# Optimization experiments

Measured on AMD Instinct MI355X. Metric: run time of the kernel, lower is better.

Reference implementation:

```python
import jax, jax.numpy as jnp
import numpy as np

N_NODES = 100000
N_EDGES = 1200000
N_GRAPHS = 512
N_REL = 3
NUM_SHAPES = 16
NUM_COLORS = 16
NUM_CLASS = 10


def setup_inputs() -> dict:
    key = jax.random.key(0)
    ks = jax.random.split(key, 16)
    inp = {
        "x": jax.random.randint(ks[0], (N_NODES, 2), 0, NUM_SHAPES),
        "edge_index": jax.random.randint(ks[1], (2, N_EDGES), 0, N_NODES),
        "edge_type": jax.random.randint(ks[2], (N_EDGES,), 0, N_REL),
        "batch": jnp.sort(jax.random.randint(ks[3], (N_NODES,), 0, N_GRAPHS)),
        # parameters
        "se": jax.random.normal(ks[4], (NUM_SHAPES, 8), jnp.float32) * 0.1,
        "ce": jax.random.normal(ks[5], (NUM_COLORS, 8), jnp.float32) * 0.1,
        "pre_w": jax.random.normal(ks[6], (16, 32), jnp.float32) * 0.1,
        "pre_b": jnp.zeros((32,), jnp.float32),
        "w1": jax.random.normal(ks[7], (N_REL, 32, 64), jnp.float32) * 0.1,
        "root1": jax.random.normal(ks[8], (32, 64), jnp.float32) * 0.1,
        "b1": jnp.zeros((64,), jnp.float32),
        "w2": jax.random.normal(ks[9], (N_REL, 64, 64), jnp.float32) * 0.1,
        "root2": jax.random.normal(ks[10], (64, 64), jnp.float32) * 0.1,
        "b2": jnp.zeros((64,), jnp.float32),
        "cls_w": jax.random.normal(ks[11], (64, NUM_CLASS), jnp.float32) * 0.1,
        "cls_b": jnp.zeros((NUM_CLASS,), jnp.float32),
    }
    return inp


def _rgcn(h, src, dst, edge_type, weight, root, bias):
    # PyG RGCNConv with aggr='mean': out = x @ root + bias + sum_r mean_{edges of rel r}(x_j @ W_r)
    out = h @ root + bias
    for r in range(N_REL):
        mask = (edge_type == r)
        hr = h @ weight[r]                      # [N, out] transform-then-gather
        msg = jnp.where(mask[:, None], hr[src], 0.0)  # [E, out]
        agg = jax.ops.segment_sum(msg, dst, num_segments=N_NODES)
        cnt = jax.ops.segment_sum(mask.astype(h.dtype), dst, num_segments=N_NODES)
        out = out + agg / jnp.maximum(cnt, 1.0)[:, None]
    return out


def reference(x, edge_index, edge_type, batch, se, ce, pre_w, pre_b,
              w1, root1, b1, w2, root2, b2, cls_w, cls_b):
    h = jnp.concatenate([se[x[:, 0]], ce[x[:, 1]]], axis=1)  # [N,16]
    h = jax.nn.relu(h @ pre_w + pre_b)                        # [N,32]
    src, dst = edge_index[0], edge_index[1]
    h = jax.nn.relu(_rgcn(h, src, dst, edge_type, w1, root1, b1))  # [N,64]
    h = jax.nn.relu(_rgcn(h, src, dst, edge_type, w2, root2, b2))  # [N,64]
    # global mean pool over graph ids
    s = jax.ops.segment_sum(h, batch, num_segments=N_GRAPHS)
    c = jax.ops.segment_sum(jnp.ones((h.shape[0],), h.dtype), batch, num_segments=N_GRAPHS)
    g = s / jnp.maximum(c, 1.0)[:, None]                      # [G,64]
    return g @ cls_w + cls_b                                  # [G,num_class]
```

## Files before the change

kernel.cpp:

```cpp
#include <hip/hip_runtime.h>

#define NN 100000
#define NE 1200000
#define NG 512
#define NSEG (3 * NN)
#define NC 4
#define CHUNK 1024
#define NCHUNK ((NSEG + CHUNK - 1) / CHUNK)

typedef __bf16 bf16x8 __attribute__((ext_vector_type(8)));
typedef float f32x4 __attribute__((ext_vector_type(4)));

static constexpr size_t AGG_OFF   = 0;
static constexpr size_t AGG_BYTES = (size_t)NSEG * 32 * 4;
static constexpr size_t HIST_OFF  = AGG_OFF + AGG_BYTES;
static constexpr size_t START_OFF = HIST_OFF + (size_t)NC * NSEG * 4;
static constexpr size_t END_OFF   = START_OFF + (size_t)NSEG * 4;
static constexpr size_t COFF_OFF  = END_OFF + (size_t)NSEG * 4;
static constexpr size_t CSUM_OFF  = COFF_OFF + (size_t)NSEG * 4;
static constexpr size_t ESRC_OFF  = CSUM_OFF + 4096;
static constexpr size_t H1_OFF    = ESRC_OFF + (size_t)NE * 4;
static constexpr size_t H2_OFF    = H1_OFF + (size_t)NN * 64 * 2;
static constexpr size_t WT1H_OFF  = H2_OFF + (size_t)NN * 64 * 4;
static constexpr size_t WT1L_OFF  = WT1H_OFF + 64 * 128 * 2;
static constexpr size_t WT2H_OFF  = WT1L_OFF + 64 * 128 * 2;
static constexpr size_t WT2L_OFF  = WT2H_OFF + 64 * 256 * 2;
static constexpr size_t TAB_OFF   = WT2L_OFF + 64 * 256 * 2;
static constexpr size_t CB_OFF    = TAB_OFF + 256 * 32 * 4;
static constexpr size_t RS_OFF    = ((CB_OFF + NN + 15) / 16) * 16;

__device__ __forceinline__ void async_copy16(void* lds, const void* g) {
    __builtin_amdgcn_global_load_lds(
        (const __attribute__((address_space(1))) void*)g,
        (__attribute__((address_space(3))) void*)lds, 16, 0, 0);
}

__device__ __forceinline__ void prepw_elem(const float* root, const float* w,
                                           __bf16* wh, __bf16* wl, int cin, int t) {
    int kt = 4 * cin;
    if (t >= 64 * kt) return;
    int j = t / kt, k = t % kt;
    int sidx = k / cin, kk = k % cin;
    float v = (sidx == 0) ? root[kk * 64 + j]
                          : w[((size_t)(sidx - 1) * cin + kk) * 64 + j];
    __bf16 h = (__bf16)v;
    wh[t] = h;
    wl[t] = (__bf16)(v - (float)h);
}

#define RB_BASE 488
__global__ __launch_bounds__(256)
void k_rank_prep(const int* __restrict__ ei, const int* __restrict__ et,
                 int* __restrict__ hist4, unsigned int* __restrict__ rs,
                 const int* __restrict__ x, const float* __restrict__ se,
                 const float* __restrict__ ce, const float* __restrict__ pw,
                 const float* __restrict__ pb,
                 const float* __restrict__ root1, const float* __restrict__ w1,
                 const float* __restrict__ root2, const float* __restrict__ w2,
                 __bf16* __restrict__ wh1, __bf16* __restrict__ wl1,
                 __bf16* __restrict__ wh2, __bf16* __restrict__ wl2,
                 float* __restrict__ table, unsigned char* __restrict__ cb) {
    int b = blockIdx.x, t = threadIdx.x;
    if (b >= RB_BASE) {
        int e = (b - RB_BASE) * 256 + t;
        if (e >= NE) return;
        int d = ei[NE + e];
        int r = et[e];
        int seg = r * NN + d;
        int c = e & (NC - 1);
        unsigned int rank = (unsigned int)atomicAdd(&hist4[c * NSEG + seg], 1);
        rs[e] = (rank << 19) | (unsigned int)seg;
        return;
    }
    if (b < 32) {
        prepw_elem(root1, w1, wh1, wl1, 32, b * 256 + t);
    } else if (b < 96) {
        prepw_elem(root2, w2, wh2, wl2, 64, (b - 32) * 256 + t);
    } else if (b == 96) {
        __shared__ float sW[16 * 32];
        __shared__ float sB[32];
        for (int i = t; i < 512; i += 256) sW[i] = pw[i];
        if (t < 32) sB[t] = pb[t];
        __syncthreads();
        int cmb = t, s = cmb >> 4, c = cmb & 15;
        float in[16];
#pragma unroll
        for (int k = 0; k < 8; k++) in[k] = se[s * 8 + k];
#pragma unroll
        for (int k = 0; k < 8; k++) in[8 + k] = ce[c * 8 + k];
        float acc[32];
#pragma unroll
        for (int j = 0; j < 32; j++) acc[j] = sB[j];
#pragma unroll
        for (int k = 0; k < 16; k++) {
            float hv = in[k];
#pragma unroll
            for (int j = 0; j < 32; j++) acc[j] += hv * sW[k * 32 + j];
        }
        float* o = table + (size_t)cmb * 32;
#pragma unroll
        for (int j = 0; j < 32; j += 4)
            *(float4*)(o + j) = make_float4(fmaxf(acc[j], 0.f), fmaxf(acc[j + 1], 0.f),
                                            fmaxf(acc[j + 2], 0.f), fmaxf(acc[j + 3], 0.f));
    } else {
        int n = (b - 97) * 256 + t;
        if (n < NN) cb[n] = (unsigned char)(x[2 * n] * 16 + x[2 * n + 1]);
    }
}

__global__ __launch_bounds__(256)
void k_chunksum(const int* __restrict__ hist4, int* __restrict__ csum) {
    __shared__ int s[256];
    int b = blockIdx.x, t = threadIdx.x;
    int base = b * CHUNK + t * 4;
    int sum = 0;
#pragma unroll
    for (int k = 0; k < 4; k++) {
        int i = base + k;
        if (i < NSEG) {
#pragma unroll
            for (int c = 0; c < NC; c++) sum += hist4[c * NSEG + i];
        }
    }
    s[t] = sum;
    __syncthreads();
    for (int off = 128; off > 0; off >>= 1) {
        if (t < off) s[t] += s[t + off];
        __syncthreads();
    }
    if (t == 0) csum[b] = s[0];
}

__global__ __launch_bounds__(512)
void k_chunkscan(int* __restrict__ csum) {
    __shared__ int s[512];
    int t = threadIdx.x;
    int v = (t < NCHUNK) ? csum[t] : 0;
    s[t] = v;
    __syncthreads();
    for (int off = 1; off < 512; off <<= 1) {
        int x = (t >= off) ? s[t - off] : 0;
        __syncthreads();
        s[t] += x;
        __syncthreads();
    }
    if (t < NCHUNK) csum[t] = s[t] - v;
}

__global__ __launch_bounds__(256)
void k_localscan(const int* __restrict__ hist4, const int* __restrict__ csum,
                 int* __restrict__ start, int* __restrict__ end, int* __restrict__ coff) {
    __shared__ int s[256];
    int b = blockIdx.x, t = threadIdx.x;
    int base = b * CHUNK + t * 4;
    int tot[4], cofv[4];
    int s4 = 0;
#pragma unroll
    for (int k = 0; k < 4; k++) {
        int i = base + k;
        int c0 = 0, c1 = 0, c2 = 0, c3 = 0;
        if (i < NSEG) {
            c0 = hist4[0 * NSEG + i];
            c1 = hist4[1 * NSEG + i];
            c2 = hist4[2 * NSEG + i];
            c3 = hist4[3 * NSEG + i];
        }
        tot[k] = c0 + c1 + c2 + c3;
        cofv[k] = c0 | ((c0 + c1) << 8) | ((c0 + c1 + c2) << 16);
        s4 += tot[k];
    }
    s[t] = s4;
    __syncthreads();
    for (int off = 1; off < 256; off <<= 1) {
        int x = (t >= off) ? s[t - off] : 0;
        __syncthreads();
        s[t] += x;
        __syncthreads();
    }
    int excl = s[t] - s4 + csum[b];
#pragma unroll
    for (int k = 0; k < 4; k++) {
        int i = base + k;
        if (i < NSEG) {
            start[i] = excl;
            end[i] = excl + tot[k];
            coff[i] = cofv[k];
        }
        excl += tot[k];
    }
}

__global__ __launch_bounds__(256)
void k_fill2(const int* __restrict__ ei, const unsigned char* __restrict__ cb,
             const int* __restrict__ start, const int* __restrict__ coff,
             const unsigned int* __restrict__ rs, int* __restrict__ esrc) {
    int e = blockIdx.x * 256 + threadIdx.x;
    if (e >= NE) return;
    int s = ei[e];
    unsigned int v = rs[e];
    int seg = (int)(v & 0x7FFFFu);
    int rank = (int)(v >> 19);
    int c = e & (NC - 1);
    int off = c ? ((coff[seg] >> (8 * (c - 1))) & 0xFF) : 0;
    int pos = start[seg] + off + rank;
    esrc[pos] = s | ((int)cb[s] << 17);
}

__global__ __launch_bounds__(256)
void k_gather_t(const int* __restrict__ start, const int* __restrict__ end,
                const int* __restrict__ esrc, const float* __restrict__ table,
                float* __restrict__ agg) {
    int tid = blockIdx.x * 256 + threadIdx.x;
    int seg = tid >> 3;
    int p = tid & 7;
    if (seg >= NSEG) return;
    int st = start[seg], en = end[seg];
    float4 acc = make_float4(0.f, 0.f, 0.f, 0.f);
    int i = st;
    for (; i + 4 <= en; i += 4) {
        int v0 = esrc[i], v1 = esrc[i + 1], v2 = esrc[i + 2], v3 = esrc[i + 3];
        float4 a = *(const float4*)(table + ((v0 >> 17) & 0xFF) * 32 + p * 4);
        float4 b = *(const float4*)(table + ((v1 >> 17) & 0xFF) * 32 + p * 4);
        float4 c = *(const float4*)(table + ((v2 >> 17) & 0xFF) * 32 + p * 4);
        float4 d = *(const float4*)(table + ((v3 >> 17) & 0xFF) * 32 + p * 4);
        acc.x += (a.x + b.x) + (c.x + d.x);
        acc.y += (a.y + b.y) + (c.y + d.y);
        acc.z += (a.z + b.z) + (c.z + d.z);
        acc.w += (a.w + b.w) + (c.w + d.w);
    }
    for (; i < en; i++) {
        int v = esrc[i];
        float4 a = *(const float4*)(table + ((v >> 17) & 0xFF) * 32 + p * 4);
        acc.x += a.x; acc.y += a.y; acc.z += a.z; acc.w += a.w;
    }
    int c = en - st;
    float inv = 1.f / (float)(c > 1 ? c : 1);
    acc.x *= inv; acc.y *= inv; acc.z *= inv; acc.w *= inv;
    *(float4*)(agg + (size_t)seg * 32 + p * 4) = acc;
}

__global__ __launch_bounds__(256)
void k_gather64(const int* __restrict__ start, const int* __restrict__ end,
                const int* __restrict__ esrc, const __bf16* __restrict__ h,
                __bf16* __restrict__ agg) {
    int tid = blockIdx.x * 256 + threadIdx.x;
    int seg = tid >> 3;
    int p = tid & 7;
    if (seg >= NSEG) return;
    int st = start[seg], en = end[seg];
    float acc[8];
#pragma unroll
    for (int j = 0; j < 8; j++) acc[j] = 0.f;
    int i = st;
    for (; i + 4 <= en; i += 4) {
        int s0 = esrc[i] & 0x1FFFF, s1 = esrc[i + 1] & 0x1FFFF;
        int s2 = esrc[i + 2] & 0x1FFFF, s3 = esrc[i + 3] & 0x1FFFF;
        bf16x8 v0 = *(const bf16x8*)(h + (size_t)s0 * 64 + p * 8);
        bf16x8 v1 = *(const bf16x8*)(h + (size_t)s1 * 64 + p * 8);
        bf16x8 v2 = *(const bf16x8*)(h + (size_t)s2 * 64 + p * 8);
        bf16x8 v3 = *(const bf16x8*)(h + (size_t)s3 * 64 + p * 8);
#pragma unroll
        for (int j = 0; j < 8; j++)
            acc[j] += ((float)v0[j] + (float)v1[j]) + ((float)v2[j] + (float)v3[j]);
    }
    for (; i < en; i++) {
        int s = esrc[i] & 0x1FFFF;
        bf16x8 v = *(const bf16x8*)(h + (size_t)s * 64 + p * 8);
#pragma unroll
        for (int j = 0; j < 8; j++) acc[j] += (float)v[j];
    }
    int c = en - st;
    float inv = 1.f / (float)(c > 1 ? c : 1);
    bf16x8 o;
#pragma unroll
    for (int j = 0; j < 8; j++) o[j] = (__bf16)(acc[j] * inv);
    *(bf16x8*)(agg + (size_t)seg * 64 + p * 8) = o;
}

__device__ __forceinline__ void split8(float4 a0, float4 a1, bf16x8& hi, bf16x8& lo) {
    float v[8] = {a0.x, a0.y, a0.z, a0.w, a1.x, a1.y, a1.z, a1.w};
#pragma unroll
    for (int i = 0; i < 8; i++) {
        __bf16 h = (__bf16)v[i];
        hi[i] = h;
        lo[i] = (__bf16)(v[i] - (float)h);
    }
}

__global__ __launch_bounds__(256, 1)
void k_combine_l1(const float* __restrict__ table, const unsigned char* __restrict__ cb,
                  const float* __restrict__ agg,
                  const __bf16* __restrict__ wh, const __bf16* __restrict__ wl,
                  const float* __restrict__ bias, __bf16* __restrict__ h_out) {
    constexpr int KT = 128;
    __shared__ float sIN[64 * 64];
    __shared__ __bf16 sWH[64 * 64];
    __shared__ __bf16 sWL[64 * 64];

    const int tid = threadIdx.x;
    const int wave = tid >> 6;
    const int lane = tid & 63;
    const int cA = lane & 15;
    const int kg = lane >> 4;
    const int n0 = blockIdx.x * 64;

    f32x4 acc[4];
#pragma unroll
    for (int nb = 0; nb < 4; nb++) {
        float bv = bias[nb * 16 + cA];
        acc[nb][0] = bv; acc[nb][1] = bv; acc[nb][2] = bv; acc[nb][3] = bv;
    }

    for (int c = 0; c < 2; c++) {
        if (c) __syncthreads();
#pragma unroll
        for (int i = 0; i < 4; i++) {
            int F = tid + i * 256;
            int row = F >> 4, j = F & 15;
            int jor = j ^ (row & 7);
            int n = n0 + row; if (n > NN - 1) n = NN - 1;
            int sidx = 2 * c + (jor >> 3);
            int jj = jor & 7;
            const float* src = (sidx == 0)
                ? table + (size_t)cb[n] * 32 + jj * 4
                : agg + ((size_t)(sidx - 1) * NN + n) * 32 + jj * 4;
            async_copy16(sIN + (size_t)F * 4, src);
        }
#pragma unroll
        for (int i = 0; i < 2; i++) {
            int F = tid + i * 256;
            int col = F >> 3, s = F & 7;
            int sor = s ^ (col & 7);
            async_copy16(sWH + (size_t)F * 8, wh + (size_t)col * KT + c * 64 + sor * 8);
            async_copy16(sWL + (size_t)F * 8, wl + (size_t)col * KT + c * 64 + sor * 8);
        }
        __syncthreads();
#pragma unroll
        for (int ks = 0; ks < 2; ks++) {
            const int rowL = wave * 16 + cA;
            const int jA = ks * 8 + kg * 2;
            float4 a0 = ((const float4*)sIN)[rowL * 16 + (jA ^ (rowL & 7))];
            float4 a1 = ((const float4*)sIN)[rowL * 16 + ((jA + 1) ^ (rowL & 7))];
            bf16x8 ah, al;
            split8(a0, a1, ah, al);
            const int k8 = ks * 4 + kg;
#pragma unroll
            for (int nb = 0; nb < 4; nb++) {
                const int col = nb * 16 + cA;
                const int bs = col * 8 + (k8 ^ (col & 7));
                bf16x8 bh = ((const bf16x8*)sWH)[bs];
                bf16x8 bl = ((const bf16x8*)sWL)[bs];
                acc[nb] = __builtin_amdgcn_mfma_f32_16x16x32_bf16(ah, bh, acc[nb], 0, 0, 0);
                acc[nb] = __builtin_amdgcn_mfma_f32_16x16x32_bf16(al, bh, acc[nb], 0, 0, 0);
                acc[nb] = __builtin_amdgcn_mfma_f32_16x16x32_bf16(ah, bl, acc[nb], 0, 0, 0);
                acc[nb] = __builtin_amdgcn_mfma_f32_16x16x32_bf16(al, bl, acc[nb], 0, 0, 0);
            }
        }
    }
#pragma unroll
    for (int nb = 0; nb < 4; nb++) {
#pragma unroll
        for (int r = 0; r < 4; r++) {
            int n = n0 + wave * 16 + kg * 4 + r;
            if (n < NN)
                h_out[(size_t)n * 64 + nb * 16 + cA] = (__bf16)fmaxf(acc[nb][r], 0.f);
        }
    }
}

__global__ __launch_bounds__(256, 1)
void k_combine_l2(const __bf16* __restrict__ h1b, const __bf16* __restrict__ aggb,
                  const __bf16* __restrict__ wh, const __bf16* __restrict__ wl,
                  const float* __restrict__ bias, float* __restrict__ h_out) {
    constexpr int KT = 256;
    __shared__ __bf16 sINb[64 * 64];
    __shared__ __bf16 sWH[64 * 64];
    __shared__ __bf16 sWL[64 * 64];

    const int tid = threadIdx.x;
    const int wave = tid >> 6;
    const int lane = tid & 63;
    const int cA = lane & 15;
    const int kg = lane >> 4;
    const int n0 = blockIdx.x * 64;

    f32x4 acc[4];
#pragma unroll
    for (int nb = 0; nb < 4; nb++) {
        float bv = bias[nb * 16 + cA];
        acc[nb][0] = bv; acc[nb][1] = bv; acc[nb][2] = bv; acc[nb][3] = bv;
    }

    for (int c = 0; c < 4; c++) {
        if (c) __syncthreads();
#pragma unroll
        for (int i = 0; i < 2; i++) {
            int F = tid + i * 256;
            int row = F >> 3, j = F & 7;
            int jor = j ^ (row & 7);
            int n = n0 + row; if (n > NN - 1) n = NN - 1;
            const __bf16* src = (c == 0)
                ? h1b + (size_t)n * 64 + jor * 8
                : aggb + ((size_t)(c - 1) * NN + n) * 64 + jor * 8;
            async_copy16(sINb + (size_t)F * 8, src);
        }
#pragma unroll
        for (int i = 0; i < 2; i++) {
            int F = tid + i * 256;
            int col = F >> 3, s = F & 7;
            int sor = s ^ (col & 7);
            async_copy16(sWH + (size_t)F * 8, wh + (size_t)col * KT + c * 64 + sor * 8);
            async_copy16(sWL + (size_t)F * 8, wl + (size_t)col * KT + c * 64 + sor * 8);
        }
        __syncthreads();
#pragma unroll
        for (int ks = 0; ks < 2; ks++) {
            const int rowL = wave * 16 + cA;
            const int s8 = ks * 4 + kg;
            bf16x8 ah = ((const bf16x8*)sINb)[rowL * 8 + (s8 ^ (rowL & 7))];
#pragma unroll
            for (int nb = 0; nb < 4; nb++) {
                const int col = nb * 16 + cA;
                const int bs = col * 8 + (s8 ^ (col & 7));
                bf16x8 bh = ((const bf16x8*)sWH)[bs];
                bf16x8 bl = ((const bf16x8*)sWL)[bs];
                acc[nb] = __builtin_amdgcn_mfma_f32_16x16x32_bf16(ah, bh, acc[nb], 0, 0, 0);
                acc[nb] = __builtin_amdgcn_mfma_f32_16x16x32_bf16(ah, bl, acc[nb], 0, 0, 0);
            }
        }
    }
#pragma unroll
    for (int nb = 0; nb < 4; nb++) {
#pragma unroll
        for (int r = 0; r < 4; r++) {
            int n = n0 + wave * 16 + kg * 4 + r;
            if (n < NN)
                h_out[(size_t)n * 64 + nb * 16 + cA] = fmaxf(acc[nb][r], 0.f);
        }
    }
}

__global__ __launch_bounds__(256)
void k_pool_final(const float* __restrict__ h, const int* __restrict__ batch,
                  const float* __restrict__ cw, const float* __restrict__ cbias,
                  float* __restrict__ out) {
    int g = blockIdx.x;
    auto lb = [&](int v) {
        int lo = 0, hi = NN;
        while (lo < hi) {
            int m = (lo + hi) >> 1;
            if (batch[m] < v) lo = m + 1; else hi = m;
        }
        return lo;
    };
    int st = lb(g), en = lb(g + 1);
    int col = threadIdx.x & 63, chunk = threadIdx.x >> 6;
    float acc = 0.f;
    for (int n = st + chunk; n < en; n += 4) acc += h[(size_t)n * 64 + col];
    __shared__ float s[256];
    __shared__ float mean[64];
    s[threadIdx.x] = acc;
    __syncthreads();
    if (chunk == 0) {
        float tot = s[col] + s[64 + col] + s[128 + col] + s[192 + col];
        int c = en - st;
        mean[col] = tot / (float)(c > 1 ? c : 1);
    }
    __syncthreads();
    if (threadIdx.x < 10) {
        int j = threadIdx.x;
        float o = cbias[j];
#pragma unroll
        for (int k = 0; k < 64; k++) o += mean[k] * cw[k * 10 + j];
        out[g * 10 + j] = o;
    }
}

extern "C" void kernel_launch(void* const* d_in, const int* in_sizes, int n_in,
                              void* d_out, int out_size, void* d_ws, size_t ws_size,
                              hipStream_t stream) {
    const int* x      = (const int*)d_in[0];
    const int* ei     = (const int*)d_in[1];
    const int* et     = (const int*)d_in[2];
    const int* batch  = (const int*)d_in[3];
    const float* se   = (const float*)d_in[4];
    const float* ce   = (const float*)d_in[5];
    const float* pw   = (const float*)d_in[6];
    const float* pb   = (const float*)d_in[7];
    const float* w1   = (const float*)d_in[8];
    const float* root1= (const float*)d_in[9];
    const float* b1   = (const float*)d_in[10];
    const float* w2   = (const float*)d_in[11];
    const float* root2= (const float*)d_in[12];
    const float* b2   = (const float*)d_in[13];
    const float* cw   = (const float*)d_in[14];
    const float* cbias= (const float*)d_in[15];
    float* out = (float*)d_out;

    char* ws = (char*)d_ws;
    float*  agg1 = (float*)(ws + AGG_OFF);
    __bf16* aggb = (__bf16*)(ws + AGG_OFF);
    int*   hist4 = (int*)(ws + HIST_OFF);
    int*   start = (int*)(ws + START_OFF);
    int*   end   = (int*)(ws + END_OFF);
    int*   coff  = (int*)(ws + COFF_OFF);
    int*   csum  = (int*)(ws + CSUM_OFF);
    int*   esrc  = (int*)(ws + ESRC_OFF);
    __bf16* h1b  = (__bf16*)(ws + H1_OFF);
    float* h2    = (float*)(ws + H2_OFF);
    __bf16* wt1h = (__bf16*)(ws + WT1H_OFF);
    __bf16* wt1l = (__bf16*)(ws + WT1L_OFF);
    __bf16* wt2h = (__bf16*)(ws + WT2H_OFF);
    __bf16* wt2l = (__bf16*)(ws + WT2L_OFF);
    float* table = (float*)(ws + TAB_OFF);
    unsigned char* cbarr = (unsigned char*)(ws + CB_OFF);
    unsigned int* rs = (unsigned int*)(ws + RS_OFF);

    (void)hipMemsetAsync(hist4, 0, (size_t)NC * NSEG * 4, stream);

    int rank_blocks = RB_BASE + (NE + 255) / 256;
    k_rank_prep<<<rank_blocks, 256, 0, stream>>>(ei, et, hist4, rs,
                                                 x, se, ce, pw, pb, root1, w1, root2, w2,
                                                 wt1h, wt1l, wt2h, wt2l, table, cbarr);

    k_chunksum<<<NCHUNK, 256, 0, stream>>>(hist4, csum);
    k_chunkscan<<<1, 512, 0, stream>>>(csum);
    k_localscan<<<NCHUNK, 256, 0, stream>>>(hist4, csum, start, end, coff);
    k_fill2<<<(NE + 255) / 256, 256, 0, stream>>>(ei, cbarr, start, coff, rs, esrc);

    k_gather_t<<<(NSEG * 8 + 255) / 256, 256, 0, stream>>>(start, end, esrc, table, agg1);
    k_combine_l1<<<(NN + 63) / 64, 256, 0, stream>>>(table, cbarr, agg1,
                                                     wt1h, wt1l, b1, h1b);
    k_gather64<<<(NSEG * 8 + 255) / 256, 256, 0, stream>>>(start, end, esrc, h1b, aggb);
    k_combine_l2<<<(NN + 63) / 64, 256, 0, stream>>>(h1b, aggb,
                                                     wt2h, wt2l, b2, h2);

    k_pool_final<<<NG, 256, 0, stream>>>(h2, batch, cw, cbias, out);
}
```

Measured before the change: 198.2 us.

## Partition edge-rank histogram per XCD and use workgroup-scope atomics

The edge ranking histogram is now split into eight copies indexed by the hardware XCC id read via s_getreg, replacing the four copies chosen by edge index. Atomics use relaxed workgroup scope so they can stay in the per-XCD L2 and skip device-wide coherence traffic. Prefix offsets per copy widen to 64-bit packed bytes and the rank field shrinks to leave room for the XCD id. This doubles the histogram memset and the scan reads. It also depends on workgroup-scope atomics being correct across workgroups on the same XCD, and on no copy of a segment exceeding 255 entries.

New measurement: 206.9 us. +4.4%, slower.

```diff
diff --git a/kernel.cpp b/kernel.cpp
--- a/kernel.cpp
+++ b/kernel.cpp
@@ -4,7 +4,7 @@
 #define NE 1200000
 #define NG 512
 #define NSEG (3 * NN)
-#define NC 4
+#define NXCD 8
 #define CHUNK 1024
 #define NCHUNK ((NSEG + CHUNK - 1) / CHUNK)
 
@@ -14,10 +14,10 @@
 static constexpr size_t AGG_OFF   = 0;
 static constexpr size_t AGG_BYTES = (size_t)NSEG * 32 * 4;
 static constexpr size_t HIST_OFF  = AGG_OFF + AGG_BYTES;
-static constexpr size_t START_OFF = HIST_OFF + (size_t)NC * NSEG * 4;
+static constexpr size_t START_OFF = HIST_OFF + (size_t)NXCD * NSEG * 4;
 static constexpr size_t END_OFF   = START_OFF + (size_t)NSEG * 4;
 static constexpr size_t COFF_OFF  = END_OFF + (size_t)NSEG * 4;
-static constexpr size_t CSUM_OFF  = COFF_OFF + (size_t)NSEG * 4;
+static constexpr size_t CSUM_OFF  = COFF_OFF + (size_t)NSEG * 8;
 static constexpr size_t ESRC_OFF  = CSUM_OFF + 4096;
 static constexpr size_t H1_OFF    = ESRC_OFF + (size_t)NE * 4;
 static constexpr size_t H2_OFF    = H1_OFF + (size_t)NN * 64 * 2;
@@ -51,7 +51,7 @@
 #define RB_BASE 488
 __global__ __launch_bounds__(256)
 void k_rank_prep(const int* __restrict__ ei, const int* __restrict__ et,
-                 int* __restrict__ hist4, unsigned int* __restrict__ rs,
+                 int* __restrict__ hist8, unsigned int* __restrict__ rs,
                  const int* __restrict__ x, const float* __restrict__ se,
                  const float* __restrict__ ce, const float* __restrict__ pw,
                  const float* __restrict__ pb,
@@ -67,9 +67,12 @@
         int d = ei[NE + e];
         int r = et[e];
         int seg = r * NN + d;
-        int c = e & (NC - 1);
-        unsigned int rank = (unsigned int)atomicAdd(&hist4[c * NSEG + seg], 1);
-        rs[e] = (rank << 19) | (unsigned int)seg;
+        unsigned int xcc;
+        asm volatile("s_getreg_b32 %0, hwreg(HW_REG_XCC_ID, 0, 32)" : "=s"(xcc));
+        int c = (int)(xcc & 7);
+        int rank = __hip_atomic_fetch_add(&hist8[c * NSEG + seg], 1,
+                                          __ATOMIC_RELAXED, __HIP_MEMORY_SCOPE_WORKGROUP);
+        rs[e] = ((unsigned int)rank << 22) | ((unsigned int)c << 19) | (unsigned int)seg;
         return;
     }
     if (b < 32) {
@@ -109,7 +112,7 @@
 }
 
 __global__ __launch_bounds__(256)
-void k_chunksum(const int* __restrict__ hist4, int* __restrict__ csum) {
+void k_chunksum(const int* __restrict__ hist8, int* __restrict__ csum) {
     __shared__ int s[256];
     int b = blockIdx.x, t = threadIdx.x;
     int base = b * CHUNK + t * 4;
@@ -119,7 +122,7 @@
         int i = base + k;
         if (i < NSEG) {
 #pragma unroll
-            for (int c = 0; c < NC; c++) sum += hist4[c * NSEG + i];
+            for (int c = 0; c < NXCD; c++) sum += hist8[c * NSEG + i];
         }
     }
     s[t] = sum;
@@ -148,26 +151,35 @@
 }
 
 __global__ __launch_bounds__(256)
-void k_localscan(const int* __restrict__ hist4, const int* __restrict__ csum,
-                 int* __restrict__ start, int* __restrict__ end, int* __restrict__ coff) {
+void k_localscan(const int* __restrict__ hist8, const int* __restrict__ csum,
+                 int* __restrict__ start, int* __restrict__ end,
+                 unsigned long long* __restrict__ coff) {
     __shared__ int s[256];
     int b = blockIdx.x, t = threadIdx.x;
     int base = b * CHUNK + t * 4;
-    int tot[4], cofv[4];
+    int tot[4];
+    unsigned long long cofv[4];
     int s4 = 0;
 #pragma unroll
     for (int k = 0; k < 4; k++) {
         int i = base + k;
-        int c0 = 0, c1 = 0, c2 = 0, c3 = 0;
+        int run = 0;
+        unsigned long long cof = 0;
         if (i < NSEG) {
-            c0 = hist4[0 * NSEG + i];
-            c1 = hist4[1 * NSEG + i];
-            c2 = hist4[2 * NSEG + i];
-            c3 = hist4[3 * NSEG + i];
-        }
-        tot[k] = c0 + c1 + c2 + c3;
-        cofv[k] = c0 | ((c0 + c1) << 8) | ((c0 + c1 + c2) << 16);
-        s4 += tot[k];
+#pragma unroll
+            for (int c = 0; c < NXCD; c++) {
+                int cnt = hist8[c * NSEG + i];
+                if (c < 7) {
+                    run += cnt;
+                    cof |= (unsigned long long)(run & 0xFF) << (8 * c);
+                } else {
+                    run += cnt;
+                }
+            }
+        }
+        tot[k] = run;
+        cofv[k] = cof;
+        s4 += run;
     }
     s[t] = s4;
     __syncthreads();
@@ -192,16 +204,16 @@
 
 __global__ __launch_bounds__(256)
 void k_fill2(const int* __restrict__ ei, const unsigned char* __restrict__ cb,
-             const int* __restrict__ start, const int* __restrict__ coff,
+             const int* __restrict__ start, const unsigned long long* __restrict__ coff,
              const unsigned int* __restrict__ rs, int* __restrict__ esrc) {
     int e = blockIdx.x * 256 + threadIdx.x;
     if (e >= NE) return;
     int s = ei[e];
     unsigned int v = rs[e];
     int seg = (int)(v & 0x7FFFFu);
-    int rank = (int)(v >> 19);
-    int c = e & (NC - 1);
-    int off = c ? ((coff[seg] >> (8 * (c - 1))) & 0xFF) : 0;
+    int c = (int)((v >> 19) & 7u);
+    int rank = (int)(v >> 22);
+    int off = c ? (int)((coff[seg] >> (8 * (c - 1))) & 0xFF) : 0;
     int pos = start[seg] + off + rank;
     esrc[pos] = s | ((int)cb[s] << 17);
 }
@@ -500,10 +512,10 @@
     char* ws = (char*)d_ws;
     float*  agg1 = (float*)(ws + AGG_OFF);
     __bf16* aggb = (__bf16*)(ws + AGG_OFF);
-    int*   hist4 = (int*)(ws + HIST_OFF);
+    int*   hist8 = (int*)(ws + HIST_OFF);
     int*   start = (int*)(ws + START_OFF);
     int*   end   = (int*)(ws + END_OFF);
-    int*   coff  = (int*)(ws + COFF_OFF);
+    unsigned long long* coff = (unsigned long long*)(ws + COFF_OFF);
     int*   csum  = (int*)(ws + CSUM_OFF);
     int*   esrc  = (int*)(ws + ESRC_OFF);
     __bf16* h1b  = (__bf16*)(ws + H1_OFF);
@@ -516,16 +528,16 @@
     unsigned char* cbarr = (unsigned char*)(ws + CB_OFF);
     unsigned int* rs = (unsigned int*)(ws + RS_OFF);
 
-    (void)hipMemsetAsync(hist4, 0, (size_t)NC * NSEG * 4, stream);
+    (void)hipMemsetAsync(hist8, 0, (size_t)NXCD * NSEG * 4, stream);
 
     int rank_blocks = RB_BASE + (NE + 255) / 256;
-    k_rank_prep<<<rank_blocks, 256, 0, stream>>>(ei, et, hist4, rs,
+    k_rank_prep<<<rank_blocks, 256, 0, stream>>>(ei, et, hist8, rs,
                                                  x, se, ce, pw, pb, root1, w1, root2, w2,
                                                  wt1h, wt1l, wt2h, wt2l, table, cbarr);
 
-    k_chunksum<<<NCHUNK, 256, 0, stream>>>(hist4, csum);
+    k_chunksum<<<NCHUNK, 256, 0, stream>>>(hist8, csum);
     k_chunkscan<<<1, 512, 0, stream>>>(csum);
-    k_localscan<<<NCHUNK, 256, 0, stream>>>(hist4, csum, start, end, coff);
+    k_localscan<<<NCHUNK, 256, 0, stream>>>(hist8, csum, start, end, coff);
     k_fill2<<<(NE + 255) / 256, 256, 0, stream>>>(ei, cbarr, start, coff, rs, esrc);
 
     k_gather_t<<<(NSEG * 8 + 255) / 256, 256, 0, stream>>>(start, end, esrc, table, agg1);
```
